# Kernel tuning notes

Measured on AMD Instinct MI355X. Metric: run time of the kernel, lower is better.

Reference implementation:

```python
import jax, jax.numpy as jnp
import numpy as np

D_MODEL = 1024
HIDDEN = 1024
N_EXPERTS = 8
TOP_K = 2
BATCH, SEQ = 2, 2048
N_TOKENS = BATCH * SEQ


def setup_inputs() -> dict:
    key = jax.random.key(0)
    ks = jax.random.split(key, 6)
    x = jax.random.normal(ks[0], (BATCH, SEQ, D_MODEL), dtype=jnp.float32)
    expert_weights = jax.random.uniform(ks[1], (N_TOKENS, TOP_K), dtype=jnp.float32)
    expert_indices = jax.random.randint(ks[2], (N_TOKENS, TOP_K), 0, N_EXPERTS, dtype=jnp.int32)
    s_in = 1.0 / np.sqrt(D_MODEL)
    s_hid = 1.0 / np.sqrt(HIDDEN)
    w1 = jax.random.normal(ks[3], (N_EXPERTS, D_MODEL, HIDDEN), dtype=jnp.float32) * s_in
    w3 = jax.random.normal(ks[4], (N_EXPERTS, D_MODEL, HIDDEN), dtype=jnp.float32) * s_in
    w2 = jax.random.normal(ks[5], (N_EXPERTS, HIDDEN, D_MODEL), dtype=jnp.float32) * s_hid
    return {"x": x, "expert_weights": expert_weights, "expert_indices": expert_indices,
            "w1": w1, "w3": w3, "w2": w2}


def reference(x, expert_weights, expert_indices, w1, w3, w2):
    """Dropless MoE MLP (forward_once path): for each token t,
    out[t] = sum_k expert_weights[t,k] * SwiGLU_{expert_indices[t,k]}(x[t]).
    Also returns batch_size_per_expert (histogram of routed assignments).
    """
    d = x.shape[-1]
    xf = x.reshape(-1, d)                                  # [N, d]
    E = w1.shape[0]
    # combine[t, e] = sum over top-k slots routed to expert e of their weight
    onehot = jax.nn.one_hot(expert_indices, E, dtype=xf.dtype)       # [N, K, E]
    combine = jnp.einsum("nk,nke->ne", expert_weights, onehot)      # [N, E]
    out = jnp.zeros_like(xf)
    for e in range(E):  # fixed small loop over experts
        h = jax.nn.silu(xf @ w1[e]) * (xf @ w3[e])          # [N, H]
        out = out + combine[:, e:e + 1] * (h @ w2[e])       # [N, d]
    batch_size_per_expert = jnp.zeros((E,), dtype=jnp.int32).at[
        expert_indices.reshape(-1)].add(1)
    return out.reshape(x.shape), batch_size_per_expert
```

## Files before the change

### kernel.cpp

```cpp
#include <hip/hip_runtime.h>
#include <cstdint>

#define D 1024
#define N_TOKENS 4096
#define N_SLOTS 8192
#define NEXP 8
#define NKT 16
#define MAXT 80

typedef float f32x4 __attribute__((ext_vector_type(4)));
typedef __bf16 bf16x8 __attribute__((ext_vector_type(8)));
typedef __attribute__((address_space(3))) uint32_t lds_u32;
typedef __attribute__((address_space(1))) const uint32_t glb_u32;

__device__ __forceinline__ void gload_lds16(const void* g, void* l) {
  __builtin_amdgcn_global_load_lds((glb_u32*)g, (lds_u32*)l, 16, 0, 0);
}

__device__ __forceinline__ ushort f2bf(float f) {
  union { float f; uint32_t u; } c; c.f = f;
  uint32_t u = c.u;
  return (ushort)((u + 0x7FFFu + ((u >> 16) & 1u)) >> 16);
}

__device__ __forceinline__ float bf2f(ushort u) {
  union { uint32_t u; float f; } c; c.u = (uint32_t)u << 16;
  return c.f;
}

__device__ __forceinline__ bf16x8 lds_frag(const ushort* base, int row, int s) {
  return *(const bf16x8*)((const char*)base + row * 128 + ((s ^ (row & 7)) * 16));
}

__global__ void prep_k(const float* __restrict__ x, const int* __restrict__ ei,
                       const float* __restrict__ ew,
                       const float* __restrict__ w1, const float* __restrict__ w3,
                       const float* __restrict__ w2,
                       float* __restrict__ hist_out, int* __restrict__ meta,
                       int* __restrict__ tok, int* __restrict__ smap,
                       ushort* __restrict__ Xbf, ushort* __restrict__ w13t,
                       ushort* __restrict__ w2t) {
  int bid = blockIdx.x, t = threadIdx.x;
  if (bid == 0) {
    __shared__ int cmat[256][8];
    __shared__ int off[NEXP + 1];
#pragma unroll
    for (int e = 0; e < NEXP; e++) cmat[t][e] = 0;
    int base = t * 32;
#pragma unroll 4
    for (int j = 0; j < 32; j++) cmat[t][ei[base + j]]++;
    __syncthreads();
    if (t < NEXP) {
      int run = 0;
      for (int i = 0; i < 256; i++) { int v = cmat[i][t]; cmat[i][t] = run; run += v; }
      meta[8 + t] = run;
    }
    __syncthreads();
    if (t == 0) {
      int s = 0;
      for (int e = 0; e < NEXP; e++) { off[e] = s; s += meta[8 + e]; }
      off[NEXP] = s;
      int nt = 0;
      for (int e = 0; e < NEXP; e++)
        for (int r = off[e]; r < off[e + 1]; r += 128)
          if (nt < MAXT) {
            meta[16 + nt] = e;
            meta[96 + nt] = r;
            int re = off[e + 1]; if (r + 128 < re) re = r + 128;
            meta[176 + nt] = re;
            nt++;
          }
      meta[0] = nt;
      for (int e = 0; e < NEXP; e++) hist_out[e] = (float)meta[8 + e];
    }
    __syncthreads();
#pragma unroll 4
    for (int j = 0; j < 32; j++) {
      int slot = base + j;
      int e = ei[slot];
      int p = off[e] + cmat[t][e]++;
      tok[p] = slot >> 1;
      smap[slot] = p;
    }
  } else if (bid <= 256) {
    int cb = bid - 1;
    const float4* xs = (const float4*)x + (size_t)cb * 4096;
    ushort4* xd = (ushort4*)Xbf + (size_t)cb * 4096;
#pragma unroll
    for (int i = 0; i < 16; i++) {
      float4 v = xs[i * 256 + t];
      ushort4 o;
      o.x = f2bf(v.x); o.y = f2bf(v.y); o.z = f2bf(v.z); o.w = f2bf(v.w);
      xd[i * 256 + t] = o;
    }
  } else {
    int wb = bid - 257;
    int z = wb >> 8, rem = wb & 255;
    int kb = rem >> 4, nb = rem & 15;
    int which = z >> 3, e = z & 7;
    const float* src = (which == 0 ? w1 : which == 1 ? w3 : w2) + (size_t)e * D * D;
    ushort* dst = (which == 2) ? (w2t + (size_t)e * D * D)
                               : (w13t + (size_t)e * 2048 * D);
    __shared__ ushort tile[64][72];
    int k0 = kb * 64, n0 = nb * 64;
    int r = t >> 4, c = t & 15;
#pragma unroll
    for (int rep = 0; rep < 4; rep++) {
      int krow = rep * 16 + r;
      float4 v = *(const float4*)(src + (size_t)(k0 + krow) * D + n0 + c * 4);
      tile[krow][c * 4 + 0] = f2bf(v.x);
      tile[krow][c * 4 + 1] = f2bf(v.y);
      tile[krow][c * 4 + 2] = f2bf(v.z);
      tile[krow][c * 4 + 3] = f2bf(v.w);
    }
    __syncthreads();
#pragma unroll
    for (int rep = 0; rep < 4; rep++) {
      int lr = rep * 16 + r;
      int nrow = n0 + lr;
      ushort4 o;
      o.x = tile[c * 4 + 0][lr];
      o.y = tile[c * 4 + 1][lr];
      o.z = tile[c * 4 + 2][lr];
      o.w = tile[c * 4 + 3][lr];
      int crow = (which == 2) ? nrow
               : ((nrow >> 4) << 5) + ((which == 1) ? 16 : 0) + (nrow & 15);
      *(ushort4*)(dst + (size_t)crow * D + k0 + c * 4) = o;
    }
  }
}

__global__ __launch_bounds__(256, 4) void gemm1_k(
    const ushort* __restrict__ Xbf, const ushort* __restrict__ W13t,
    ushort* __restrict__ H, const int* __restrict__ tok,
    const int* __restrict__ meta) {
  int tm = blockIdx.y;
  if (tm >= meta[0]) return;
  int e = meta[16 + tm], r0 = meta[96 + tm], rend = meta[176 + tm];
  int n0i = blockIdx.x * 128;
  int tid = threadIdx.x, lane = tid & 63, wid = tid >> 6;
  int wm = wid >> 1, wn = wid & 1;

  __shared__ ushort sA[128 * 64];
  __shared__ ushort sB[128 * 64];

  const char* gX = (const char*)Xbf;
  const char* gB = (const char*)(W13t + (size_t)e * 2048 * D);

  int prow = tid >> 3, pslot = tid & 7;
  size_t arow[4];
  int brow[4];
#pragma unroll
  for (int i = 0; i < 4; i++) {
    int row = i * 32 + prow;
    int gr = r0 + row; if (gr > N_SLOTS - 1) gr = N_SLOTS - 1;
    arow[i] = (size_t)tok[gr] * 2048;
    brow[i] = n0i + row;
  }

  f32x4 acc[4][4] = {};

  for (int kt = 0; kt < NKT; kt++) {
    int kb = kt * 128;
#pragma unroll
    for (int i = 0; i < 4; i++) {
      int row = i * 32 + prow;
      int phys = (pslot ^ (row & 7)) * 16;
      gload_lds16(gX + arow[i] + kb + phys, (char*)sA + (i * 256 + tid) * 16);
      gload_lds16(gB + (size_t)brow[i] * 2048 + kb + phys,
                  (char*)sB + (i * 256 + tid) * 16);
    }
    __syncthreads();
#pragma unroll
    for (int kk = 0; kk < 2; kk++) {
      int s = kk * 4 + (lane >> 4);
      bf16x8 a[4], b[4];
#pragma unroll
      for (int mf = 0; mf < 4; mf++)
        a[mf] = lds_frag(sA, wm * 64 + mf * 16 + (lane & 15), s);
#pragma unroll
      for (int nf = 0; nf < 4; nf++)
        b[nf] = lds_frag(sB, wn * 64 + nf * 16 + (lane & 15), s);
#pragma unroll
      for (int mf = 0; mf < 4; mf++)
#pragma unroll
        for (int nf = 0; nf < 4; nf++)
          acc[mf][nf] = __builtin_amdgcn_mfma_f32_16x16x32_bf16(a[mf], b[nf], acc[mf][nf], 0, 0, 0);
    }
    __syncthreads();
  }

  int cb = (n0i >> 1) + wn * 32 + (lane & 15);
#pragma unroll
  for (int mf = 0; mf < 4; mf++)
#pragma unroll
    for (int v = 0; v < 4; v++) {
      int r = r0 + wm * 64 + mf * 16 + (lane >> 4) * 4 + v;
      if (r >= rend) continue;
#pragma unroll
      for (int p = 0; p < 2; p++) {
        float g = acc[mf][2 * p][v], u = acc[mf][2 * p + 1][v];
        float hv = g / (1.f + __expf(-g)) * u;
        H[(size_t)r * D + cb + p * 16] = f2bf(hv);
      }
    }
}

__global__ __launch_bounds__(256, 4) void gemm2_k(
    const ushort* __restrict__ Hm, const ushort* __restrict__ W2t,
    ushort* __restrict__ Y, const int* __restrict__ meta) {
  int tm = blockIdx.y;
  if (tm >= meta[0]) return;
  int e = meta[16 + tm], r0 = meta[96 + tm], rend = meta[176 + tm];
  int n0 = blockIdx.x * 64;
  int tid = threadIdx.x, lane = tid & 63, wid = tid >> 6;
  int wm = wid >> 1, wn = wid & 1;

  __shared__ ushort sA[128 * 64];
  __shared__ ushort sB[64 * 64];

  const char* gH = (const char*)Hm;
  const char* gB = (const char*)(W2t + (size_t)e * D * D);

  int prow = tid >> 3, pslot = tid & 7;
  size_t arow[4];
#pragma unroll
  for (int i = 0; i < 4; i++) {
    int row = i * 32 + prow;
    int gr = r0 + row; if (gr > N_SLOTS - 1) gr = N_SLOTS - 1;
    arow[i] = (size_t)gr * 2048;
  }

  f32x4 acc[4][2] = {};

  for (int kt = 0; kt < NKT; kt++) {
    int kb = kt * 128;
#pragma unroll
    for (int i = 0; i < 4; i++) {
      int row = i * 32 + prow;
      int phys = (pslot ^ (row & 7)) * 16;
      gload_lds16(gH + arow[i] + kb + phys, (char*)sA + (i * 256 + tid) * 16);
    }
#pragma unroll
    for (int i = 0; i < 2; i++) {
      int row = i * 32 + prow;
      int phys = (pslot ^ (row & 7)) * 16;
      gload_lds16(gB + (size_t)(n0 + row) * 2048 + kb + phys,
                  (char*)sB + (i * 256 + tid) * 16);
    }
    __syncthreads();
#pragma unroll
    for (int kk = 0; kk < 2; kk++) {
      int s = kk * 4 + (lane >> 4);
      bf16x8 a[4], b[2];
#pragma unroll
      for (int mf = 0; mf < 4; mf++)
        a[mf] = lds_frag(sA, wm * 64 + mf * 16 + (lane & 15), s);
#pragma unroll
      for (int nf = 0; nf < 2; nf++)
        b[nf] = lds_frag(sB, wn * 32 + nf * 16 + (lane & 15), s);
#pragma unroll
      for (int mf = 0; mf < 4; mf++)
#pragma unroll
        for (int nf = 0; nf < 2; nf++)
          acc[mf][nf] = __builtin_amdgcn_mfma_f32_16x16x32_bf16(a[mf], b[nf], acc[mf][nf], 0, 0, 0);
    }
    __syncthreads();
  }

#pragma unroll
  for (int mf = 0; mf < 4; mf++)
#pragma unroll
    for (int v = 0; v < 4; v++) {
      int r = r0 + wm * 64 + mf * 16 + (lane >> 4) * 4 + v;
      if (r >= rend) continue;
#pragma unroll
      for (int nf = 0; nf < 2; nf++)
        Y[(size_t)r * D + n0 + wn * 32 + nf * 16 + (lane & 15)] = f2bf(acc[mf][nf][v]);
    }
}

__global__ void combine_k(const ushort* __restrict__ Y, const int* __restrict__ smap,
                          const float* __restrict__ ew, float* __restrict__ out) {
  int tkn = blockIdx.x * 4 + (threadIdx.x >> 6);
  int lane = threadIdx.x & 63;
  int p0 = smap[2 * tkn], p1 = smap[2 * tkn + 1];
  float w0 = ew[2 * tkn], w1 = ew[2 * tkn + 1];
  const ushort4* y0 = (const ushort4*)(Y + (size_t)p0 * D);
  const ushort4* y1 = (const ushort4*)(Y + (size_t)p1 * D);
  float4* o = (float4*)(out + (size_t)tkn * D);
#pragma unroll
  for (int j = 0; j < 4; j++) {
    int c = j * 64 + lane;
    ushort4 a = y0[c], b = y1[c];
    float4 v;
    v.x = w0 * bf2f(a.x) + w1 * bf2f(b.x);
    v.y = w0 * bf2f(a.y) + w1 * bf2f(b.y);
    v.z = w0 * bf2f(a.z) + w1 * bf2f(b.z);
    v.w = w0 * bf2f(a.w) + w1 * bf2f(b.w);
    o[c] = v;
  }
}

extern "C" void kernel_launch(void* const* d_in, const int* in_sizes, int n_in,
                              void* d_out, int out_size, void* d_ws, size_t ws_size,
                              hipStream_t stream) {
  const float* x  = (const float*)d_in[0];
  const float* ew = (const float*)d_in[1];
  const int*   ei = (const int*)d_in[2];
  const float* w1 = (const float*)d_in[3];
  const float* w3 = (const float*)d_in[4];
  const float* w2 = (const float*)d_in[5];
  float* out = (float*)d_out;

  char* ws = (char*)d_ws;
  int*    meta = (int*)ws;
  int*    tok  = (int*)(ws + 4096);
  int*    smap = (int*)(ws + 4096 + 32768);
  ushort* Xbf  = (ushort*)(ws + (1ull << 20));
  ushort* W13t = (ushort*)(ws + (9ull << 20));
  ushort* W2t  = (ushort*)(ws + (41ull << 20));
  ushort* Hm   = (ushort*)(ws + (57ull << 20));
  ushort* Ym   = (ushort*)(ws + (1ull << 20));

  prep_k<<<6401, 256, 0, stream>>>(x, ei, ew, w1, w3, w2,
                                   out + (size_t)N_TOKENS * D, meta, tok, smap,
                                   Xbf, W13t, W2t);
  gemm1_k<<<dim3(16, MAXT), 256, 0, stream>>>(Xbf, W13t, Hm, tok, meta);
  gemm2_k<<<dim3(16, MAXT), 256, 0, stream>>>(Hm, W2t, Ym, meta);
  combine_k<<<N_TOKENS / 4, 256, 0, stream>>>(Ym, smap, ew, out);
}
```

Measured before the change: 118.8 us.

## Double-buffer GEMM tiles, widen gemm2 N tile, move W2 conversion into gemm1

Both expert GEMMs now stage K tiles into double-buffered LDS through async global-to-LDS loads, waiting with partial vmcnt so the next tile's loads overlap the MFMAs on the current one. gemm2's N tile grows from 64 to 128 so each block reuses its A tile across more columns, with half as many blocks. The W2 fp32-to-bf16 transpose leaves the prep kernel and runs in 128 extra gemm1 blocks, overlapping it with GEMM1 work. LDS per block doubles and occupancy bounds drop from 4 to 2 blocks per CU. The extra gemm1 blocks each loop over 16 tiles serially, which could leave a long tail.

```diff
diff --git a/kernel.cpp b/kernel.cpp
--- a/kernel.cpp
+++ b/kernel.cpp
@@ -35,11 +35,9 @@
 __global__ void prep_k(const float* __restrict__ x, const int* __restrict__ ei,
                        const float* __restrict__ ew,
                        const float* __restrict__ w1, const float* __restrict__ w3,
-                       const float* __restrict__ w2,
                        float* __restrict__ hist_out, int* __restrict__ meta,
                        int* __restrict__ tok, int* __restrict__ smap,
-                       ushort* __restrict__ Xbf, ushort* __restrict__ w13t,
-                       ushort* __restrict__ w2t) {
+                       ushort* __restrict__ Xbf, ushort* __restrict__ w13t) {
   int bid = blockIdx.x, t = threadIdx.x;
   if (bid == 0) {
     __shared__ int cmat[256][8];
@@ -98,9 +96,8 @@
     int z = wb >> 8, rem = wb & 255;
     int kb = rem >> 4, nb = rem & 15;
     int which = z >> 3, e = z & 7;
-    const float* src = (which == 0 ? w1 : which == 1 ? w3 : w2) + (size_t)e * D * D;
-    ushort* dst = (which == 2) ? (w2t + (size_t)e * D * D)
-                               : (w13t + (size_t)e * 2048 * D);
+    const float* src = (which == 0 ? w1 : w3) + (size_t)e * D * D;
+    ushort* dst = w13t + (size_t)e * 2048 * D;
     __shared__ ushort tile[64][72];
     int k0 = kb * 64, n0 = nb * 64;
     int r = t >> 4, c = t & 15;
@@ -123,71 +120,119 @@
       o.y = tile[c * 4 + 1][lr];
       o.z = tile[c * 4 + 2][lr];
       o.w = tile[c * 4 + 3][lr];
-      int crow = (which == 2) ? nrow
-               : ((nrow >> 4) << 5) + ((which == 1) ? 16 : 0) + (nrow & 15);
+      int crow = ((nrow >> 4) << 5) + ((which == 1) ? 16 : 0) + (nrow & 15);
       *(ushort4*)(dst + (size_t)crow * D + k0 + c * 4) = o;
     }
   }
 }
 
-__global__ __launch_bounds__(256, 4) void gemm1_k(
+#define STAGE_TILE(sAb, sBb, kb_) do {                                        \
+  int kb = (kb_);                                                             \
+  _Pragma("unroll")                                                           \
+  for (int i = 0; i < 4; i++) {                                               \
+    gload_lds16(gA + arow[i] + kb + phys[i],                                  \
+                (char*)(sAb) + (i * 256 + tid) * 16);                         \
+    gload_lds16(gB + (size_t)brow[i] * 2048 + kb + phys[i],                   \
+                (char*)(sBb) + (i * 256 + tid) * 16);                         \
+  } } while (0)
+
+__global__ __launch_bounds__(256, 2) void gemm1_k(
     const ushort* __restrict__ Xbf, const ushort* __restrict__ W13t,
     ushort* __restrict__ H, const int* __restrict__ tok,
-    const int* __restrict__ meta) {
+    const int* __restrict__ meta,
+    const float* __restrict__ w2, ushort* __restrict__ W2t) {
+  __shared__ ushort sA[2][128 * 64];
+  __shared__ ushort sB[2][128 * 64];
   int tm = blockIdx.y;
+  int tid = threadIdx.x;
+
+  if (tm >= MAXT) {
+    int e = tm - MAXT;
+    const float* src = w2 + (size_t)e * D * D;
+    ushort* dst = W2t + (size_t)e * D * D;
+    ushort (*tile)[72] = (ushort(*)[72]) & sA[0][0];
+    int kb = blockIdx.x;
+    int r = tid >> 4, c = tid & 15;
+    int k0 = kb * 64;
+    for (int nb = 0; nb < 16; nb++) {
+      int n0 = nb * 64;
+      __syncthreads();
+#pragma unroll
+      for (int rep = 0; rep < 4; rep++) {
+        int krow = rep * 16 + r;
+        float4 v = *(const float4*)(src + (size_t)(k0 + krow) * D + n0 + c * 4);
+        tile[krow][c * 4 + 0] = f2bf(v.x);
+        tile[krow][c * 4 + 1] = f2bf(v.y);
+        tile[krow][c * 4 + 2] = f2bf(v.z);
+        tile[krow][c * 4 + 3] = f2bf(v.w);
+      }
+      __syncthreads();
+#pragma unroll
+      for (int rep = 0; rep < 4; rep++) {
+        int lr = rep * 16 + r;
+        ushort4 o;
+        o.x = tile[c * 4 + 0][lr];
+        o.y = tile[c * 4 + 1][lr];
+        o.z = tile[c * 4 + 2][lr];
+        o.w = tile[c * 4 + 3][lr];
+        *(ushort4*)(dst + (size_t)(n0 + lr) * D + k0 + c * 4) = o;
+      }
+    }
+    return;
+  }
   if (tm >= meta[0]) return;
+
   int e = meta[16 + tm], r0 = meta[96 + tm], rend = meta[176 + tm];
   int n0i = blockIdx.x * 128;
-  int tid = threadIdx.x, lane = tid & 63, wid = tid >> 6;
+  int lane = tid & 63, wid = tid >> 6;
   int wm = wid >> 1, wn = wid & 1;
 
-  __shared__ ushort sA[128 * 64];
-  __shared__ ushort sB[128 * 64];
-
-  const char* gX = (const char*)Xbf;
+  const char* gA = (const char*)Xbf;
   const char* gB = (const char*)(W13t + (size_t)e * 2048 * D);
 
   int prow = tid >> 3, pslot = tid & 7;
   size_t arow[4];
-  int brow[4];
+  int brow[4], phys[4];
 #pragma unroll
   for (int i = 0; i < 4; i++) {
     int row = i * 32 + prow;
     int gr = r0 + row; if (gr > N_SLOTS - 1) gr = N_SLOTS - 1;
     arow[i] = (size_t)tok[gr] * 2048;
     brow[i] = n0i + row;
+    phys[i] = (pslot ^ (row & 7)) * 16;
   }
 
   f32x4 acc[4][4] = {};
 
+  STAGE_TILE(&sA[0][0], &sB[0][0], 0);
+  int cur = 0;
   for (int kt = 0; kt < NKT; kt++) {
-    int kb = kt * 128;
-#pragma unroll
-    for (int i = 0; i < 4; i++) {
-      int row = i * 32 + prow;
-      int phys = (pslot ^ (row & 7)) * 16;
-      gload_lds16(gX + arow[i] + kb + phys, (char*)sA + (i * 256 + tid) * 16);
-      gload_lds16(gB + (size_t)brow[i] * 2048 + kb + phys,
-                  (char*)sB + (i * 256 + tid) * 16);
-    }
-    __syncthreads();
+    if (kt + 1 < NKT) {
+      STAGE_TILE(&sA[cur ^ 1][0], &sB[cur ^ 1][0], (kt + 1) * 128);
+      asm volatile("s_waitcnt vmcnt(8)" ::: "memory");
+    } else {
+      asm volatile("s_waitcnt vmcnt(0)" ::: "memory");
+    }
+    __builtin_amdgcn_s_barrier();
 #pragma unroll
     for (int kk = 0; kk < 2; kk++) {
       int s = kk * 4 + (lane >> 4);
       bf16x8 a[4], b[4];
 #pragma unroll
       for (int mf = 0; mf < 4; mf++)
-        a[mf] = lds_frag(sA, wm * 64 + mf * 16 + (lane & 15), s);
+        a[mf] = lds_frag(&sA[cur][0], wm * 64 + mf * 16 + (lane & 15), s);
 #pragma unroll
       for (int nf = 0; nf < 4; nf++)
-        b[nf] = lds_frag(sB, wn * 64 + nf * 16 + (lane & 15), s);
+        b[nf] = lds_frag(&sB[cur][0], wn * 64 + nf * 16 + (lane & 15), s);
 #pragma unroll
       for (int mf = 0; mf < 4; mf++)
 #pragma unroll
         for (int nf = 0; nf < 4; nf++)
           acc[mf][nf] = __builtin_amdgcn_mfma_f32_16x16x32_bf16(a[mf], b[nf], acc[mf][nf], 0, 0, 0);
     }
-    __syncthreads();
+    __builtin_amdgcn_s_barrier();
+    __builtin_amdgcn_sched_barrier(0);
+    cur ^= 1;
   }
 
   int cb = (n0i >> 1) + wn * 32 + (lane & 15);
@@ -206,66 +251,64 @@
     }
 }
 
-__global__ __launch_bounds__(256, 4) void gemm2_k(
+__global__ __launch_bounds__(256, 2) void gemm2_k(
     const ushort* __restrict__ Hm, const ushort* __restrict__ W2t,
     ushort* __restrict__ Y, const int* __restrict__ meta) {
+  __shared__ ushort sA[2][128 * 64];
+  __shared__ ushort sB[2][128 * 64];
   int tm = blockIdx.y;
   if (tm >= meta[0]) return;
   int e = meta[16 + tm], r0 = meta[96 + tm], rend = meta[176 + tm];
-  int n0 = blockIdx.x * 64;
+  int n0 = blockIdx.x * 128;
   int tid = threadIdx.x, lane = tid & 63, wid = tid >> 6;
   int wm = wid >> 1, wn = wid & 1;
 
-  __shared__ ushort sA[128 * 64];
-  __shared__ ushort sB[64 * 64];
-
-  const char* gH = (const char*)Hm;
+  const char* gA = (const char*)Hm;
   const char* gB = (const char*)(W2t + (size_t)e * D * D);
 
   int prow = tid >> 3, pslot = tid & 7;
   size_t arow[4];
+  int brow[4], phys[4];
 #pragma unroll
   for (int i = 0; i < 4; i++) {
     int row = i * 32 + prow;
     int gr = r0 + row; if (gr > N_SLOTS - 1) gr = N_SLOTS - 1;
     arow[i] = (size_t)gr * 2048;
-  }
-
-  f32x4 acc[4][2] = {};
-
+    brow[i] = n0 + row;
+    phys[i] = (pslot ^ (row & 7)) * 16;
+  }
+
+  f32x4 acc[4][4] = {};
+
+  STAGE_TILE(&sA[0][0], &sB[0][0], 0);
+  int cur = 0;
   for (int kt = 0; kt < NKT; kt++) {
-    int kb = kt * 128;
-#pragma unroll
-    for (int i = 0; i < 4; i++) {
-      int row = i * 32 + prow;
-      int phys = (pslot ^ (row & 7)) * 16;
-      gload_lds16(gH + arow[i] + kb + phys, (char*)sA + (i * 256 + tid) * 16);
-    }
-#pragma unroll
-    for (int i = 0; i < 2; i++) {
-      int row = i * 32 + prow;
-      int phys = (pslot ^ (row & 7)) * 16;
-      gload_lds16(gB + (size_t)(n0 + row) * 2048 + kb + phys,
-                  (char*)sB + (i * 256 + tid) * 16);
-    }
-    __syncthreads();
+    if (kt + 1 < NKT) {
+      STAGE_TILE(&sA[cur ^ 1][0], &sB[cur ^ 1][0], (kt + 1) * 128);
+      asm volatile("s_waitcnt vmcnt(8)" ::: "memory");
+    } else {
+      asm volatile("s_waitcnt vmcnt(0)" ::: "memory");
+    }
+    __builtin_amdgcn_s_barrier();
 #pragma unroll
     for (int kk = 0; kk < 2; kk++) {
       int s = kk * 4 + (lane >> 4);
-      bf16x8 a[4], b[2];
+      bf16x8 a[4], b[4];
 #pragma unroll
       for (int mf = 0; mf < 4; mf++)
-        a[mf] = lds_frag(sA, wm * 64 + mf * 16 + (lane & 15), s);
-#pragma unroll
-      for (int nf = 0; nf < 2; nf++)
-        b[nf] = lds_frag(sB, wn * 32 + nf * 16 + (lane & 15), s);
+        a[mf] = lds_frag(&sA[cur][0], wm * 64 + mf * 16 + (lane & 15), s);
+#pragma unroll
+      for (int nf = 0; nf < 4; nf++)
+        b[nf] = lds_frag(&sB[cur][0], wn * 64 + nf * 16 + (lane & 15), s);
 #pragma unroll
       for (int mf = 0; mf < 4; mf++)
 #pragma unroll
-        for (int nf = 0; nf < 2; nf++)
+        for (int nf = 0; nf < 4; nf++)
           acc[mf][nf] = __builtin_amdgcn_mfma_f32_16x16x32_bf16(a[mf], b[nf], acc[mf][nf], 0, 0, 0);
     }
-    __syncthreads();
+    __builtin_amdgcn_s_barrier();
+    __builtin_amdgcn_sched_barrier(0);
+    cur ^= 1;
   }
 
 #pragma unroll
@@ -275,8 +318,8 @@
       int r = r0 + wm * 64 + mf * 16 + (lane >> 4) * 4 + v;
       if (r >= rend) continue;
 #pragma unroll
-      for (int nf = 0; nf < 2; nf++)
-        Y[(size_t)r * D + n0 + wn * 32 + nf * 16 + (lane & 15)] = f2bf(acc[mf][nf][v]);
+      for (int nf = 0; nf < 4; nf++)
+        Y[(size_t)r * D + n0 + wn * 64 + nf * 16 + (lane & 15)] = f2bf(acc[mf][nf][v]);
     }
 }
 
@@ -323,10 +366,10 @@
   ushort* Hm   = (ushort*)(ws + (57ull << 20));
   ushort* Ym   = (ushort*)(ws + (1ull << 20));
 
-  prep_k<<<6401, 256, 0, stream>>>(x, ei, ew, w1, w3, w2,
+  prep_k<<<4353, 256, 0, stream>>>(x, ei, ew, w1, w3,
                                    out + (size_t)N_TOKENS * D, meta, tok, smap,
-                                   Xbf, W13t, W2t);
-  gemm1_k<<<dim3(16, MAXT), 256, 0, stream>>>(Xbf, W13t, Hm, tok, meta);
-  gemm2_k<<<dim3(16, MAXT), 256, 0, stream>>>(Hm, W2t, Ym, meta);
+                                   Xbf, W13t);
+  gemm1_k<<<dim3(16, MAXT + 8), 256, 0, stream>>>(Xbf, W13t, Hm, tok, meta, w2, W2t);
+  gemm2_k<<<dim3(8, MAXT), 256, 0, stream>>>(Hm, W2t, Ym, meta);
   combine_k<<<N_TOKENS / 4, 256, 0, stream>>>(Ym, smap, ew, out);
 }
```

Measured after the change: 136.8 us. 1.15x slower.
